# Kernel optimization log

Hardware: AMD Instinct MI355X
Metric: run time of the kernel (lower is better)

## Reference

```python
import jax, jax.numpy as jnp
import numpy as np

N = 10000      # nodes
E = 320000     # edges (before self-loops)
IN_DIM = 128
HID = 64
OUT = 32
HEADS = 8
NEG_SLOPE = 0.2  # PyG GATConv default leaky_relu slope


def gat_conv(x, W, a_src, a_dst, b, src, dst, num_nodes, heads, d):
    """One PyG-style GATConv layer (eval mode, concat=True).
    x: [N, F_in], W: [F_in, heads*d], a_src/a_dst: [heads, d], b: [heads*d]
    src/dst: [E'] int edge endpoints (self-loops already included).
    """
    h = (x @ W).reshape(num_nodes, heads, d)              # [N, H, D]
    alpha_s = jnp.sum(h * a_src, axis=-1)                 # [N, H]
    alpha_d = jnp.sum(h * a_dst, axis=-1)                 # [N, H]
    logits = jax.nn.leaky_relu(alpha_s[src] + alpha_d[dst], NEG_SLOPE)  # [E', H]
    # segment softmax over incoming edges of each destination node
    m = jax.lax.stop_gradient(
        jax.ops.segment_max(logits, dst, num_segments=num_nodes))      # [N, H]
    e = jnp.exp(logits - m[dst])                          # [E', H]
    denom = jax.ops.segment_sum(e, dst, num_segments=num_nodes)        # [N, H]
    alpha = e / denom[dst]                                # [E', H]
    out = jax.ops.segment_sum(alpha[:, :, None] * h[src], dst,
                              num_segments=num_nodes)     # [N, H, D]
    return out.reshape(num_nodes, heads * d) + b


def setup_inputs() -> dict:
    key = jax.random.key(0)
    ks = jax.random.split(key, 10)
    x = jax.random.normal(ks[0], (N, IN_DIM), jnp.float32)
    edge_index = jax.random.randint(ks[1], (2, E), 0, N, dtype=jnp.int64)
    s1 = 1.0 / np.sqrt(IN_DIM)
    W1 = jax.random.normal(ks[2], (IN_DIM, HEADS * HID), jnp.float32) * s1
    a1_src = jax.random.normal(ks[3], (HEADS, HID), jnp.float32) * 0.1
    a1_dst = jax.random.normal(ks[4], (HEADS, HID), jnp.float32) * 0.1
    b1 = jnp.zeros((HEADS * HID,), jnp.float32)
    s2 = 1.0 / np.sqrt(HEADS * HID)
    W2 = jax.random.normal(ks[5], (HEADS * HID, OUT), jnp.float32) * s2
    a2_src = jax.random.normal(ks[6], (1, OUT), jnp.float32) * 0.1
    a2_dst = jax.random.normal(ks[7], (1, OUT), jnp.float32) * 0.1
    b2 = jnp.zeros((OUT,), jnp.float32)
    return {"x": x, "edge_index": edge_index,
            "W1": W1, "a1_src": a1_src, "a1_dst": a1_dst, "b1": b1,
            "W2": W2, "a2_src": a2_src, "a2_dst": a2_dst, "b2": b2}


def reference(x, edge_index, W1, a1_src, a1_dst, b1, W2, a2_src, a2_dst, b2):
    # add self-loops (PyG GATConv default add_self_loops=True)
    loops = jnp.arange(N, dtype=edge_index.dtype)
    src = jnp.concatenate([edge_index[0], loops])
    dst = jnp.concatenate([edge_index[1], loops])
    # dropout layers are identity in eval mode
    h = gat_conv(x, W1, a1_src, a1_dst, b1, src, dst, N, HEADS, HID)
    h = jax.nn.elu(h)
    out = gat_conv(h, W2, a2_src, a2_dst, b2, src, dst, N, 1, OUT)
    return out
```

## Files before the change

### kernel.cpp

```cpp
#include <hip/hip_runtime.h>
#include <math.h>

#define N_NODES 10000
#define E_EDGES 320000
#define EA      (E_EDGES + N_NODES)
#define IN_DIM  128
#define HID     512
#define HEADS   8
#define OUT_DIM 32
#define NEG     0.2f
#define CAP     160
#define N_PAD   10048
#define NRB     628
#define RB_SH   4096

#define PWB  32
#define ZBK  40
#define SCB  645

typedef __attribute__((ext_vector_type(8))) short bf16x8;
typedef __attribute__((ext_vector_type(4))) float f32x4;

__device__ __forceinline__ float leaky(float x){ return x > 0.f ? x : NEG * x; }

__device__ __forceinline__ unsigned short bf16rn(float x){
    unsigned int b = __float_as_uint(x);
    b += 0x7fffu + ((b >> 16) & 1u);
    return (unsigned short)(b >> 16);
}

__global__ void k_pre(const float* __restrict__ x, const float* __restrict__ W1,
                      int* __restrict__ cnt,
                      unsigned short* __restrict__ Ax, unsigned short* __restrict__ Bt){
    int b = blockIdx.x, t = threadIdx.x;
    if (b < NRB){
        __shared__ float xs[16 * 132];
        int rb = b;
#pragma unroll
        for (int j = 0; j < 2; j++){
            int idx = t + j * 256;
            int r = idx >> 5, c4 = idx & 31;
            int row = rb * 16 + r;
            float4 v = make_float4(0.f, 0.f, 0.f, 0.f);
            if (row < N_NODES)
                v = *reinterpret_cast<const float4*>(x + (size_t)row * IN_DIM + c4 * 4);
            *reinterpret_cast<float4*>(&xs[r * 132 + c4 * 4]) = v;
        }
        __syncthreads();
        int l15 = t & 15, kk8 = t >> 4;
        unsigned short hi[8], lo[8];
#pragma unroll
        for (int el = 0; el < 8; el++){
            float f = xs[l15 * 132 + kk8 * 8 + el];
            hi[el] = bf16rn(f);
            lo[el] = bf16rn(f - __uint_as_float((unsigned)hi[el] << 16));
        }
        uint4 H, L;
        H.x = hi[0] | ((unsigned)hi[1] << 16); H.y = hi[2] | ((unsigned)hi[3] << 16);
        H.z = hi[4] | ((unsigned)hi[5] << 16); H.w = hi[6] | ((unsigned)hi[7] << 16);
        L.x = lo[0] | ((unsigned)lo[1] << 16); L.y = lo[2] | ((unsigned)lo[3] << 16);
        L.z = lo[4] | ((unsigned)lo[5] << 16); L.w = lo[6] | ((unsigned)lo[7] << 16);
        unsigned short* base = Ax + (size_t)rb * RB_SH;
        *reinterpret_cast<uint4*>(base + (kk8 * 16 + l15) * 8) = H;
        *reinterpret_cast<uint4*>(base + 2048 + (kk8 * 16 + l15) * 8) = L;
    } else if (b < NRB + PWB){
        __shared__ float wsh[128 * 17];
        int nb = b - NRB;
        int j = t & 15, kr = t >> 4;
#pragma unroll
        for (int it = 0; it < 8; it++){
            int k = it * 16 + kr;
            wsh[k * 17 + j] = W1[(size_t)k * HID + nb * 16 + j];
        }
        __syncthreads();
        int l15 = t & 15, kk8 = t >> 4;
        unsigned short hi[8], lo[8];
#pragma unroll
        for (int el = 0; el < 8; el++){
            float f = wsh[(kk8 * 8 + el) * 17 + l15];
            hi[el] = bf16rn(f);
            lo[el] = bf16rn(f - __uint_as_float((unsigned)hi[el] << 16));
        }
        uint4 H, L;
        H.x = hi[0] | ((unsigned)hi[1] << 16); H.y = hi[2] | ((unsigned)hi[3] << 16);
        H.z = hi[4] | ((unsigned)hi[5] << 16); H.w = hi[6] | ((unsigned)hi[7] << 16);
        L.x = lo[0] | ((unsigned)lo[1] << 16); L.y = lo[2] | ((unsigned)lo[3] << 16);
        L.z = lo[4] | ((unsigned)lo[5] << 16); L.w = lo[6] | ((unsigned)lo[7] << 16);
        unsigned short* base = Bt + (size_t)nb * RB_SH;
        *reinterpret_cast<uint4*>(base + (kk8 * 16 + l15) * 8) = H;
        *reinterpret_cast<uint4*>(base + 2048 + (kk8 * 16 + l15) * 8) = L;
    } else {
        int i = (b - NRB - PWB) * 256 + t;
        if (i < N_NODES) cnt[i] = 0;
    }
}

__launch_bounds__(512)
__global__ void k_sg(const int* __restrict__ eidx, int* __restrict__ cnt,
                     int* __restrict__ esrc,
                     const unsigned short* __restrict__ Ax,
                     const unsigned short* __restrict__ Bt,
                     const float* __restrict__ a1s, const float* __restrict__ a1d,
                     unsigned short* __restrict__ h1,
                     float* __restrict__ as1, float* __restrict__ ad1){
    if (blockIdx.x < SCB){
        int e = blockIdx.x * 512 + threadIdx.x;
        if (e < EA){
            int d, s;
            if (e < E_EDGES){ s = eidx[e]; d = eidx[E_EDGES + e]; }
            else { s = d = e - E_EDGES; }
            int pos = atomicAdd(&cnt[d], 1);
            if (pos < CAP) esrc[d * CAP + pos] = s;
        }
        return;
    }
    int rb = blockIdx.x - SCB;
    int by = threadIdx.x >> 6;
    int lane = threadIdx.x & 63;
    int l15 = lane & 15, grp = lane >> 4;
    int m0 = rb * 16;
    int n0 = by * 64;
    const unsigned short* ap = Ax + (size_t)rb * RB_SH + (size_t)lane * 8;
    bf16x8 a_hi[4], a_lo[4];
#pragma unroll
    for (int ks = 0; ks < 4; ks++){
        a_hi[ks] = *reinterpret_cast<const bf16x8*>(ap + ks * 512);
        a_lo[ks] = *reinterpret_cast<const bf16x8*>(ap + 2048 + ks * 512);
    }
    const unsigned short* bp = Bt + (size_t)(by * 4) * RB_SH + (size_t)lane * 8;
    f32x4 acc[4] = {};
#pragma unroll
    for (int ks = 0; ks < 4; ks++){
#pragma unroll
        for (int ns = 0; ns < 4; ns++){
            const unsigned short* bb = bp + (size_t)ns * RB_SH + ks * 512;
            bf16x8 b_hi = *reinterpret_cast<const bf16x8*>(bb);
            bf16x8 b_lo = *reinterpret_cast<const bf16x8*>(bb + 2048);
            acc[ns] = __builtin_amdgcn_mfma_f32_16x16x32_bf16(a_hi[ks], b_hi, acc[ns], 0, 0, 0);
            acc[ns] = __builtin_amdgcn_mfma_f32_16x16x32_bf16(a_lo[ks], b_hi, acc[ns], 0, 0, 0);
            acc[ns] = __builtin_amdgcn_mfma_f32_16x16x32_bf16(a_hi[ks], b_lo, acc[ns], 0, 0, 0);
        }
    }
    float vs[4] = {0.f, 0.f, 0.f, 0.f}, vd[4] = {0.f, 0.f, 0.f, 0.f};
#pragma unroll
    for (int ns = 0; ns < 4; ns++){
        int c = n0 + ns * 16 + l15;
        float a_s = a1s[c], a_d = a1d[c];
#pragma unroll
        for (int r = 0; r < 4; r++){
            float v = acc[ns][r];
            int rr = m0 + grp * 4 + r;
            if (rr < N_NODES) h1[(size_t)rr * HID + c] = bf16rn(v);
            vs[r] += v * a_s; vd[r] += v * a_d;
        }
    }
#pragma unroll
    for (int r = 0; r < 4; r++){
#pragma unroll
        for (int off = 8; off >= 1; off >>= 1){
            vs[r] += __shfl_xor(vs[r], off);
            vd[r] += __shfl_xor(vd[r], off);
        }
    }
    if (l15 == 0){
#pragma unroll
        for (int r = 0; r < 4; r++){
            int rr = m0 + grp * 4 + r;
            if (rr < N_NODES){ as1[rr * HEADS + by] = vs[r]; ad1[rr * HEADS + by] = vd[r]; }
        }
    }
}

__launch_bounds__(128)
__global__ void k_agg1(const unsigned short* __restrict__ h1,
                       const float* __restrict__ as1, const float* __restrict__ ad1,
                       const int* __restrict__ cnt, const int* __restrict__ esrc,
                       const float* __restrict__ b1, float* __restrict__ h1b){
    int n = blockIdx.x;
    int c = cnt[n]; if (c > CAP) c = CAP;
    int beg = n * CAP;
    int t = threadIdx.x;
    __shared__ int   s_src[CAP];
    __shared__ float s_w[HEADS][CAP + 1];
    __shared__ float s_adn[HEADS];
    __shared__ float s_red[2][HEADS];
    __shared__ float s_m[HEADS];
    if (t < HEADS) s_adn[t] = ad1[n * HEADS + t];
    __syncthreads();
    float pm[HEADS];
#pragma unroll
    for (int h = 0; h < HEADS; h++) pm[h] = -INFINITY;
    for (int i = t; i < c; i += 128){
        int s = esrc[beg + i];
        float4 alo = *reinterpret_cast<const float4*>(as1 + (size_t)s * HEADS);
        float4 ahi = *reinterpret_cast<const float4*>(as1 + (size_t)s * HEADS + 4);
        float lg[HEADS];
        lg[0] = leaky(alo.x + s_adn[0]); lg[1] = leaky(alo.y + s_adn[1]);
        lg[2] = leaky(alo.z + s_adn[2]); lg[3] = leaky(alo.w + s_adn[3]);
        lg[4] = leaky(ahi.x + s_adn[4]); lg[5] = leaky(ahi.y + s_adn[5]);
        lg[6] = leaky(ahi.z + s_adn[6]); lg[7] = leaky(ahi.w + s_adn[7]);
        s_src[i] = s;
#pragma unroll
        for (int h = 0; h < HEADS; h++){ s_w[h][i] = lg[h]; pm[h] = fmaxf(pm[h], lg[h]); }
    }
#pragma unroll
    for (int h = 0; h < HEADS; h++)
#pragma unroll
        for (int off = 32; off >= 1; off >>= 1)
            pm[h] = fmaxf(pm[h], __shfl_down(pm[h], off));
    int wv = t >> 6;
    if ((t & 63) == 0)
#pragma unroll
        for (int h = 0; h < HEADS; h++) s_red[wv][h] = pm[h];
    __syncthreads();
    if (t < HEADS) s_m[t] = fmaxf(s_red[0][t], s_red[1][t]);
    __syncthreads();
    for (int i = t; i < c; i += 128){
#pragma unroll
        for (int h = 0; h < HEADS; h++) s_w[h][i] = __expf(s_w[h][i] - s_m[h]);
    }
    __syncthreads();
    int d0 = 4 * t;
    int h = t >> 4;
    float a0a = 0.f, a1a = 0.f, a2a = 0.f, a3a = 0.f, dena = 0.f;
    float a0b = 0.f, a1b = 0.f, a2b = 0.f, a3b = 0.f, denb = 0.f;
    int i = 0;
    for (; i + 1 < c; i += 2){
        float wa = s_w[h][i];     int sa = s_src[i];
        float wb = s_w[h][i + 1]; int sb = s_src[i + 1];
        uint2 hva = *reinterpret_cast<const uint2*>(h1 + (size_t)sa * HID + d0);
        uint2 hvb = *reinterpret_cast<const uint2*>(h1 + (size_t)sb * HID + d0);
        a0a += wa * __uint_as_float(hva.x << 16);
        a1a += wa * __uint_as_float(hva.x & 0xffff0000u);
        a2a += wa * __uint_as_float(hva.y << 16);
        a3a += wa * __uint_as_float(hva.y & 0xffff0000u);
        dena += wa;
        a0b += wb * __uint_as_float(hvb.x << 16);
        a1b += wb * __uint_as_float(hvb.x & 0xffff0000u);
        a2b += wb * __uint_as_float(hvb.y << 16);
        a3b += wb * __uint_as_float(hvb.y & 0xffff0000u);
        denb += wb;
    }
    if (i < c){
        float w = s_w[h][i]; int s = s_src[i];
        uint2 hv = *reinterpret_cast<const uint2*>(h1 + (size_t)s * HID + d0);
        a0a += w * __uint_as_float(hv.x << 16);
        a1a += w * __uint_as_float(hv.x & 0xffff0000u);
        a2a += w * __uint_as_float(hv.y << 16);
        a3a += w * __uint_as_float(hv.y & 0xffff0000u);
        dena += w;
    }
    float acc0 = a0a + a0b, acc1 = a1a + a1b, acc2 = a2a + a2b, acc3 = a3a + a3b;
    float den = dena + denb;
    float4 bv = *reinterpret_cast<const float4*>(b1 + d0);
    float rd = 1.f / den;
    float o0 = acc0 * rd + bv.x;
    float o1 = acc1 * rd + bv.y;
    float o2 = acc2 * rd + bv.z;
    float o3 = acc3 * rd + bv.w;
    float4 o;
    o.x = o0 > 0.f ? o0 : expm1f(o0);
    o.y = o1 > 0.f ? o1 : expm1f(o1);
    o.z = o2 > 0.f ? o2 : expm1f(o2);
    o.w = o3 > 0.f ? o3 : expm1f(o3);
    *reinterpret_cast<float4*>(h1b + (size_t)n * HID + d0) = o;
}

__launch_bounds__(128)
__global__ void k_gemm2(const float* __restrict__ h1b, const float* __restrict__ W2,
                        const float* __restrict__ a2s, const float* __restrict__ a2d,
                        float* __restrict__ h2, float* __restrict__ as2,
                        float* __restrict__ ad2){
    __shared__ float hs[16 * 516];
    int t = threadIdx.x;
    int n0 = blockIdx.x * 16;
    const float4* src = reinterpret_cast<const float4*>(h1b + (size_t)n0 * HID);
    for (int i = t; i < 2048; i += 128){
        int r = i >> 7, c4 = i & 127;
        *reinterpret_cast<float4*>(&hs[r * 516 + c4 * 4]) = src[i];
    }
    __syncthreads();
    int nl = t >> 3, cg = t & 7, c0 = cg * 4;
    float a0 = 0.f, a1 = 0.f, a2 = 0.f, a3 = 0.f;
#pragma unroll 2
    for (int k4 = 0; k4 < 128; k4++){
        float4 hv = *reinterpret_cast<const float4*>(&hs[nl * 516 + k4 * 4]);
        float4 w0 = *reinterpret_cast<const float4*>(W2 + (k4 * 4 + 0) * OUT_DIM + c0);
        float4 w1 = *reinterpret_cast<const float4*>(W2 + (k4 * 4 + 1) * OUT_DIM + c0);
        float4 w2 = *reinterpret_cast<const float4*>(W2 + (k4 * 4 + 2) * OUT_DIM + c0);
        float4 w3 = *reinterpret_cast<const float4*>(W2 + (k4 * 4 + 3) * OUT_DIM + c0);
        a0 += hv.x * w0.x + hv.y * w1.x + hv.z * w2.x + hv.w * w3.x;
        a1 += hv.x * w0.y + hv.y * w1.y + hv.z * w2.y + hv.w * w3.y;
        a2 += hv.x * w0.z + hv.y * w1.z + hv.z * w2.z + hv.w * w3.z;
        a3 += hv.x * w0.w + hv.y * w1.w + hv.z * w2.w + hv.w * w3.w;
    }
    float4 o; o.x = a0; o.y = a1; o.z = a2; o.w = a3;
    *reinterpret_cast<float4*>(h2 + (size_t)(n0 + nl) * OUT_DIM + c0) = o;
    float4 s4 = *reinterpret_cast<const float4*>(a2s + c0);
    float4 d4 = *reinterpret_cast<const float4*>(a2d + c0);
    float vs = a0 * s4.x + a1 * s4.y + a2 * s4.z + a3 * s4.w;
    float vd = a0 * d4.x + a1 * d4.y + a2 * d4.z + a3 * d4.w;
#pragma unroll
    for (int off = 4; off >= 1; off >>= 1){
        vs += __shfl_xor(vs, off);
        vd += __shfl_xor(vd, off);
    }
    if (cg == 0){ as2[n0 + nl] = vs; ad2[n0 + nl] = vd; }
}

__launch_bounds__(256)
__global__ void k_agg2(const float* __restrict__ h2, const float* __restrict__ as2,
                       const float* __restrict__ ad2, const int* __restrict__ cnt,
                       const int* __restrict__ esrc,
                       const float* __restrict__ b2, float* __restrict__ out){
    int wv = threadIdx.x >> 6;
    int lane = threadIdx.x & 63;
    int n = blockIdx.x * 4 + wv;
    __shared__ float s_w[4][CAP];
    __shared__ int   s_src[4][CAP];
    int c = cnt[n]; if (c > CAP) c = CAP;
    int beg = n * CAP;
    float adn = ad2[n];
    float pm = -INFINITY;
    for (int i = lane; i < c; i += 64){
        int s = esrc[beg + i];
        float lg = leaky(as2[s] + adn);
        s_src[wv][i] = s; s_w[wv][i] = lg;
        pm = fmaxf(pm, lg);
    }
#pragma unroll
    for (int off = 32; off >= 1; off >>= 1)
        pm = fmaxf(pm, __shfl_xor(pm, off));
    __syncthreads();
    for (int i = lane; i < c; i += 64) s_w[wv][i] = __expf(s_w[wv][i] - pm);
    __syncthreads();
    int d = lane & 31, half = lane >> 5;
    float acc = 0.f, den = 0.f;
    for (int i = half; i < c; i += 2){
        float w = s_w[wv][i]; int s = s_src[wv][i];
        acc += w * h2[(size_t)s * OUT_DIM + d];
        den += w;
    }
    acc += __shfl_xor(acc, 32);
    den += __shfl_xor(den, 32);
    if (lane < OUT_DIM) out[(size_t)n * OUT_DIM + d] = acc / den + b2[d];
}

extern "C" void kernel_launch(void* const* d_in, const int* in_sizes, int n_in,
                              void* d_out, int out_size, void* d_ws, size_t ws_size,
                              hipStream_t stream){
    const float* x   = (const float*)d_in[0];
    const int*  eidx = (const int*)  d_in[1];
    const float* W1  = (const float*)d_in[2];
    const float* a1s = (const float*)d_in[3];
    const float* a1d = (const float*)d_in[4];
    const float* b1  = (const float*)d_in[5];
    const float* W2  = (const float*)d_in[6];
    const float* a2s = (const float*)d_in[7];
    const float* a2d = (const float*)d_in[8];
    const float* b2  = (const float*)d_in[9];
    float* out = (float*)d_out;

    char* ws = (char*)d_ws;
    size_t off = 0;
    auto alloc = [&](size_t bytes) -> void* {
        void* p = ws + off;
        off += (bytes + 255) & ~(size_t)255;
        return p;
    };
    unsigned short* h1 = (unsigned short*)alloc((size_t)N_NODES * HID * 2);
    float* h1b  = (float*)alloc((size_t)N_NODES * HID * 4);
    unsigned short* Bt = (unsigned short*)alloc((size_t)32 * RB_SH * 2);
    float* as1  = (float*)alloc((size_t)N_NODES * HEADS * 4);
    float* ad1  = (float*)alloc((size_t)N_NODES * HEADS * 4);
    float* h2   = (float*)alloc((size_t)N_NODES * OUT_DIM * 4);
    float* vs2  = (float*)alloc((size_t)N_NODES * 4);
    float* vd2  = (float*)alloc((size_t)N_NODES * 4);
    int* cnt    = (int*)alloc((size_t)N_NODES * 4);
    int* esrc   = (int*)alloc((size_t)N_NODES * CAP * 4);
    unsigned short* Ax = (unsigned short*)h1b;

    k_pre <<<NRB + PWB + ZBK, 256, 0, stream>>>(x, W1, cnt, Ax, Bt);
    k_sg  <<<SCB + NRB, 512, 0, stream>>>(eidx, cnt, esrc, Ax, Bt, a1s, a1d,
                                          h1, as1, ad1);
    k_agg1<<<N_NODES, 128, 0, stream>>>(h1, as1, ad1, cnt, esrc, b1, h1b);
    k_gemm2<<<N_NODES / 16, 128, 0, stream>>>(h1b, W2, a2s, a2d, h2, vs2, vd2);
    k_agg2<<<N_NODES / 4, 256, 0, stream>>>(h2, vs2, vd2, cnt, esrc, b2, out);
}
```

Before: 126.8 us.

## Split layer-1 aggregation per head across blocks and store h1 as fp16

The layer-1 aggregation kernel now launches four blocks per destination node, with each wave owning one head. Each wave computes its own logits, max and exp, and stores weights and row offsets in shared memory. Each lane gathers one fp16 element per edge instead of four bf16 elements, and h1 storage switches from bf16 to fp16. The goal is more parallelism and less redundant softmax work per thread. In exchange, gathers become narrow 2-byte loads, the edge list is read four times per node, and fp16 trades range for precision.

```diff
diff --git a/kernel.cpp b/kernel.cpp
--- a/kernel.cpp
+++ b/kernel.cpp
@@ -27,6 +27,15 @@
     unsigned int b = __float_as_uint(x);
     b += 0x7fffu + ((b >> 16) & 1u);
     return (unsigned short)(b >> 16);
+}
+
+__device__ __forceinline__ unsigned short f16bits(float x){
+    _Float16 h = (_Float16)x;
+    return __builtin_bit_cast(unsigned short, h);
+}
+
+__device__ __forceinline__ float f16val(unsigned short u){
+    return (float)__builtin_bit_cast(_Float16, u);
 }
 
 __global__ void k_pre(const float* __restrict__ x, const float* __restrict__ W1,
@@ -150,7 +159,7 @@
         for (int r = 0; r < 4; r++){
             float v = acc[ns][r];
             int rr = m0 + grp * 4 + r;
-            if (rr < N_NODES) h1[(size_t)rr * HID + c] = bf16rn(v);
+            if (rr < N_NODES) h1[(size_t)rr * HID + c] = f16bits(v);
             vs[r] += v * a_s; vd[r] += v * a_d;
         }
     }
@@ -176,94 +185,47 @@
                        const float* __restrict__ as1, const float* __restrict__ ad1,
                        const int* __restrict__ cnt, const int* __restrict__ esrc,
                        const float* __restrict__ b1, float* __restrict__ h1b){
-    int n = blockIdx.x;
+    int n  = blockIdx.x >> 2;
+    int gp = blockIdx.x & 3;
+    int w  = threadIdx.x >> 6;
+    int lane = threadIdx.x & 63;
+    int g = gp * 2 + w;
     int c = cnt[n]; if (c > CAP) c = CAP;
     int beg = n * CAP;
-    int t = threadIdx.x;
-    __shared__ int   s_src[CAP];
-    __shared__ float s_w[HEADS][CAP + 1];
-    __shared__ float s_adn[HEADS];
-    __shared__ float s_red[2][HEADS];
-    __shared__ float s_m[HEADS];
-    if (t < HEADS) s_adn[t] = ad1[n * HEADS + t];
-    __syncthreads();
-    float pm[HEADS];
-#pragma unroll
-    for (int h = 0; h < HEADS; h++) pm[h] = -INFINITY;
-    for (int i = t; i < c; i += 128){
+    __shared__ float2 s_ws[2][CAP];
+    float adn = ad1[(n << 3) + g];
+    float pm = -INFINITY;
+    for (int i = lane; i < c; i += 64){
         int s = esrc[beg + i];
-        float4 alo = *reinterpret_cast<const float4*>(as1 + (size_t)s * HEADS);
-        float4 ahi = *reinterpret_cast<const float4*>(as1 + (size_t)s * HEADS + 4);
-        float lg[HEADS];
-        lg[0] = leaky(alo.x + s_adn[0]); lg[1] = leaky(alo.y + s_adn[1]);
-        lg[2] = leaky(alo.z + s_adn[2]); lg[3] = leaky(alo.w + s_adn[3]);
-        lg[4] = leaky(ahi.x + s_adn[4]); lg[5] = leaky(ahi.y + s_adn[5]);
-        lg[6] = leaky(ahi.z + s_adn[6]); lg[7] = leaky(ahi.w + s_adn[7]);
-        s_src[i] = s;
-#pragma unroll
-        for (int h = 0; h < HEADS; h++){ s_w[h][i] = lg[h]; pm[h] = fmaxf(pm[h], lg[h]); }
-    }
-#pragma unroll
-    for (int h = 0; h < HEADS; h++)
-#pragma unroll
-        for (int off = 32; off >= 1; off >>= 1)
-            pm[h] = fmaxf(pm[h], __shfl_down(pm[h], off));
-    int wv = t >> 6;
-    if ((t & 63) == 0)
-#pragma unroll
-        for (int h = 0; h < HEADS; h++) s_red[wv][h] = pm[h];
-    __syncthreads();
-    if (t < HEADS) s_m[t] = fmaxf(s_red[0][t], s_red[1][t]);
-    __syncthreads();
-    for (int i = t; i < c; i += 128){
-#pragma unroll
-        for (int h = 0; h < HEADS; h++) s_w[h][i] = __expf(s_w[h][i] - s_m[h]);
-    }
-    __syncthreads();
-    int d0 = 4 * t;
-    int h = t >> 4;
-    float a0a = 0.f, a1a = 0.f, a2a = 0.f, a3a = 0.f, dena = 0.f;
-    float a0b = 0.f, a1b = 0.f, a2b = 0.f, a3b = 0.f, denb = 0.f;
+        float lg = leaky(as1[(s << 3) + g] + adn);
+        s_ws[w][i] = make_float2(lg, __uint_as_float((unsigned)s << 9));
+        pm = fmaxf(pm, lg);
+    }
+#pragma unroll
+    for (int off = 32; off >= 1; off >>= 1)
+        pm = fmaxf(pm, __shfl_xor(pm, off));
+    __syncthreads();
+    for (int i = lane; i < c; i += 64) s_ws[w][i].x = __expf(s_ws[w][i].x - pm);
+    __syncthreads();
+    unsigned d = (unsigned)(g * 64 + lane);
+    float acc0 = 0.f, acc1 = 0.f, den0 = 0.f, den1 = 0.f;
     int i = 0;
     for (; i + 1 < c; i += 2){
-        float wa = s_w[h][i];     int sa = s_src[i];
-        float wb = s_w[h][i + 1]; int sb = s_src[i + 1];
-        uint2 hva = *reinterpret_cast<const uint2*>(h1 + (size_t)sa * HID + d0);
-        uint2 hvb = *reinterpret_cast<const uint2*>(h1 + (size_t)sb * HID + d0);
-        a0a += wa * __uint_as_float(hva.x << 16);
-        a1a += wa * __uint_as_float(hva.x & 0xffff0000u);
-        a2a += wa * __uint_as_float(hva.y << 16);
-        a3a += wa * __uint_as_float(hva.y & 0xffff0000u);
-        dena += wa;
-        a0b += wb * __uint_as_float(hvb.x << 16);
-        a1b += wb * __uint_as_float(hvb.x & 0xffff0000u);
-        a2b += wb * __uint_as_float(hvb.y << 16);
-        a3b += wb * __uint_as_float(hvb.y & 0xffff0000u);
-        denb += wb;
+        float2 e0 = s_ws[w][i], e1 = s_ws[w][i + 1];
+        unsigned i0 = __float_as_uint(e0.y) + d;
+        unsigned i1 = __float_as_uint(e1.y) + d;
+        float f0 = f16val(h1[i0]);
+        float f1 = f16val(h1[i1]);
+        acc0 += e0.x * f0; den0 += e0.x;
+        acc1 += e1.x * f1; den1 += e1.x;
     }
     if (i < c){
-        float w = s_w[h][i]; int s = s_src[i];
-        uint2 hv = *reinterpret_cast<const uint2*>(h1 + (size_t)s * HID + d0);
-        a0a += w * __uint_as_float(hv.x << 16);
-        a1a += w * __uint_as_float(hv.x & 0xffff0000u);
-        a2a += w * __uint_as_float(hv.y << 16);
-        a3a += w * __uint_as_float(hv.y & 0xffff0000u);
-        dena += w;
-    }
-    float acc0 = a0a + a0b, acc1 = a1a + a1b, acc2 = a2a + a2b, acc3 = a3a + a3b;
-    float den = dena + denb;
-    float4 bv = *reinterpret_cast<const float4*>(b1 + d0);
-    float rd = 1.f / den;
-    float o0 = acc0 * rd + bv.x;
-    float o1 = acc1 * rd + bv.y;
-    float o2 = acc2 * rd + bv.z;
-    float o3 = acc3 * rd + bv.w;
-    float4 o;
-    o.x = o0 > 0.f ? o0 : expm1f(o0);
-    o.y = o1 > 0.f ? o1 : expm1f(o1);
-    o.z = o2 > 0.f ? o2 : expm1f(o2);
-    o.w = o3 > 0.f ? o3 : expm1f(o3);
-    *reinterpret_cast<float4*>(h1b + (size_t)n * HID + d0) = o;
+        float2 e0 = s_ws[w][i];
+        acc0 += e0.x * f16val(h1[__float_as_uint(e0.y) + d]);
+        den0 += e0.x;
+    }
+    float o = (acc0 + acc1) / (den0 + den1) + b1[d];
+    h1b[(size_t)n * HID + d] = o > 0.f ? o : expm1f(o);
 }
 
 __launch_bounds__(128)
@@ -383,7 +345,7 @@
     k_pre <<<NRB + PWB + ZBK, 256, 0, stream>>>(x, W1, cnt, Ax, Bt);
     k_sg  <<<SCB + NRB, 512, 0, stream>>>(eidx, cnt, esrc, Ax, Bt, a1s, a1d,
                                           h1, as1, ad1);
-    k_agg1<<<N_NODES, 128, 0, stream>>>(h1, as1, ad1, cnt, esrc, b1, h1b);
+    k_agg1<<<N_NODES * 4, 128, 0, stream>>>(h1, as1, ad1, cnt, esrc, b1, h1b);
     k_gemm2<<<N_NODES / 16, 128, 0, stream>>>(h1b, W2, a2s, a2d, h2, vs2, vd2);
     k_agg2<<<N_NODES / 4, 256, 0, stream>>>(h2, vs2, vd2, cnt, esrc, b2, out);
 }
```

Result: slower. 144.3 us (+13.7%).
